# Kernel optimization log

Measured on AMD Instinct MI355X. Metric: run time of the kernel, lower is better.

The kernel has to match this reference:

```python
import jax, jax.numpy as jnp
import numpy as np

N = 8192
TEMP = 0.5
EPS = 1e-12


def _normalize(z):
    # F.normalize(z, p=2, dim=1): x / max(||x||, eps)
    n = jnp.sqrt(jnp.sum(z * z, axis=1, keepdims=True))
    return z / jnp.maximum(n, EPS)


def _gcn(edge_index, edge_weight, x, w, b):
    # torch.sparse.mm(adj, x @ w): out[row] += adj[row, col] * support[col]
    support = x @ w
    msg = support[edge_index[1]] * edge_weight[:, None]
    return jax.ops.segment_sum(msg, edge_index[0], num_segments=N) + b


def _encoder(edge_index, edge_weight, feat, w_l1a, b_l1a, w_l1b, b_l1b, w_g1, b_g1, w_g2, b_g2):
    x = jax.nn.relu(feat @ w_l1a + b_l1a) @ w_l1b + b_l1b  # [N, 32]
    h = jax.nn.relu(_gcn(edge_index, edge_weight, x, w_g1, b_g1))  # [N, hid]
    return _gcn(edge_index, edge_weight, h, w_g2, b_g2)  # [N, act_fn]


def _proj(h, w_fc1, b_fc1, w_fc2, b_fc2):
    return jax.nn.elu(h @ w_fc1 + b_fc1) @ w_fc2 + b_fc2


def _loss(z1, z2):
    z1n = _normalize(z1)
    z2n = _normalize(z2)
    refl = jnp.exp((z1n @ z1n.T) / TEMP)      # [N, N]
    between = jnp.exp((z1n @ z2n.T) / TEMP)   # [N, N]
    denom = refl.sum(1) + between.sum(1) - jnp.diagonal(refl)
    return -jnp.log(jnp.diagonal(between) / denom)


def setup_inputs() -> dict:
    key = jax.random.key(0)
    ks = jax.random.split(key, 20)
    E = 262144
    in_dim, hid_dim, act_fn, out_dim = 512, 256, 128, 64

    def kaiming(k, shape):
        fan_in = shape[0]
        bound = np.sqrt(6.0 / fan_in)
        return jax.random.uniform(k, shape, jnp.float32, -bound, bound)

    return {
        "feat1": jax.random.normal(ks[0], (N, in_dim), jnp.float32),
        "feat2": jax.random.normal(ks[1], (N, in_dim), jnp.float32),
        "edge_index1": jax.random.randint(ks[2], (2, E), 0, N, jnp.int32),
        "edge_weight1": jax.random.uniform(ks[3], (E,), jnp.float32),
        "edge_index2": jax.random.randint(ks[4], (2, E), 0, N, jnp.int32),
        "edge_weight2": jax.random.uniform(ks[5], (E,), jnp.float32),
        "w_l1a": kaiming(ks[6], (in_dim, 64)),
        "b_l1a": jnp.zeros((64,), jnp.float32),
        "w_l1b": kaiming(ks[7], (64, 32)),
        "b_l1b": jnp.zeros((32,), jnp.float32),
        "w_g1": kaiming(ks[8], (32, hid_dim)),
        "b_g1": jnp.zeros((hid_dim,), jnp.float32),
        "w_g2": kaiming(ks[9], (hid_dim, act_fn)),
        "b_g2": jnp.zeros((act_fn,), jnp.float32),
        "w_fc1": kaiming(ks[10], (act_fn, out_dim)),
        "b_fc1": jnp.zeros((out_dim,), jnp.float32),
        "w_fc2": kaiming(ks[11], (out_dim, act_fn)),
        "b_fc2": jnp.zeros((act_fn,), jnp.float32),
    }


def reference(feat1, feat2, edge_index1, edge_weight1, edge_index2, edge_weight2,
              w_l1a, b_l1a, w_l1b, b_l1b, w_g1, b_g1, w_g2, b_g2,
              w_fc1, b_fc1, w_fc2, b_fc2):
    h1 = _encoder(edge_index1, edge_weight1, feat1, w_l1a, b_l1a, w_l1b, b_l1b, w_g1, b_g1, w_g2, b_g2)
    h2 = _encoder(edge_index2, edge_weight2, feat2, w_l1a, b_l1a, w_l1b, b_l1b, w_g1, b_g1, w_g2, b_g2)
    z1 = _proj(h1, w_fc1, b_fc1, w_fc2, b_fc2)
    z2 = _proj(h2, w_fc1, b_fc1, w_fc2, b_fc2)
    l1 = _loss(z1, z2)
    l2 = _loss(z2, z1)
    return ((l1 + l2) * 0.5).mean()
```

## Files before the change

### kernel.cpp

```cpp
#include <hip/hip_runtime.h>
#include <hip/hip_bf16.h>
#include <math.h>


#define NROWS 8192
#define MROWS 16384
#define NEDGE 262144

typedef __attribute__((ext_vector_type(8))) short bf16x8;
typedef __attribute__((ext_vector_type(4))) float f32x4;
typedef __attribute__((ext_vector_type(2))) float f32x2;
typedef long long i64;

__device__ __forceinline__ short f2bf(float f){
  union { float f; unsigned u; } cv; cv.f = f;
  unsigned u = cv.u;
  unsigned r = (u + 0x7fffu + ((u >> 16) & 1u)) >> 16;
  return (short)r;
}
__device__ __forceinline__ f32x4 mfma16(bf16x8 a, bf16x8 b, f32x4 c){
  return __builtin_amdgcn_mfma_f32_16x16x32_bf16(a, b, c, 0, 0, 0);
}
__device__ __forceinline__ float fexp2(float x){
#if __has_builtin(__builtin_amdgcn_exp2f)
  return __builtin_amdgcn_exp2f(x);
#else
  return exp2f(x);
#endif
}

__device__ unsigned char f2e4m3_sw(float f){
  float a = fabsf(f);
  unsigned s = (__float_as_uint(f)>>24)&0x80u;
  if (!(a>0.f)) return (unsigned char)s;
  if (a>448.f) a=448.f;
  int e; frexpf(a,&e);
  int eff=e-1;
  unsigned code;
  if (eff<-6){
    float q=rintf(a*512.f);
    code=(unsigned)q; if(code>7)code=7;
  } else {
    float q=rintf(a*exp2f((float)(3-eff)));
    unsigned mant=(unsigned)q;
    if(mant>=16){mant=8;eff++;}
    if(eff>8) return (unsigned char)(s|0x7e);
    code=((unsigned)(eff+7)<<3)|(mant-8);
  }
  return (unsigned char)(s|code);
}
__device__ __forceinline__ unsigned short pack2fp8(float a, float b){
#if __has_builtin(__builtin_amdgcn_cvt_pk_fp8_f32)
  int v = __builtin_amdgcn_cvt_pk_fp8_f32(a, b, 0, false);
  return (unsigned short)(v & 0xffff);
#else
  return (unsigned short)((unsigned)f2e4m3_sw(a) | ((unsigned)f2e4m3_sw(b)<<8));
#endif
}

struct WtArgs {
  const float* src[6];
  short* dst[6];
  int K[6], N[6];
  int off[7];
  int nwt;
};
__global__ void setup_k(WtArgs a, const int* __restrict__ ei1, const int* __restrict__ ei2,
                        int* __restrict__ deg1, int* __restrict__ deg2){
  int b = blockIdx.x;
  if (b < a.nwt){
    int i = b*256 + threadIdx.x;
    if (i >= a.off[6]) return;
    int s = 0;
    #pragma unroll
    for (int j=1;j<6;j++) if (i >= a.off[j]) s=j;
    int l = i - a.off[s];
    int K=a.K[s], N=a.N[s];
    int k=l/N, n=l-k*N;
    a.dst[s][(long)n*K+k] = f2bf(a.src[s][l]);
  } else {
    int hb = b - a.nwt;
    const int* ei = (hb < NEDGE/256) ? ei1 : ei2;
    int* deg = (hb < NEDGE/256) ? deg1 : deg2;
    int e = (hb % (NEDGE/256))*256 + threadIdx.x;
    atomicAdd(&deg[ei[e]], 1);
  }
}

__global__ __launch_bounds__(256) void mlp12_k(const float* __restrict__ F0, const float* __restrict__ F1,
                                               const short* __restrict__ Wa, const float* __restrict__ ba,
                                               const short* __restrict__ Wb, const float* __restrict__ bb,
                                               short* __restrict__ xb){
  __shared__ short As[32*520];
  __shared__ short a1s[32*72];
  const int tid = threadIdx.x;
  const int m0 = blockIdx.x*32;
  const float* F = (m0 < NROWS) ? (F0 + (long)m0*512) : (F1 + (long)(m0-NROWS)*512);
  {
    float4 st[16];
    #pragma unroll
    for (int i=0;i<16;i++) st[i] = *(const float4*)(F + (long)(i*256+tid)*4);
    #pragma unroll
    for (int i=0;i<16;i++){
      int idx = i*256+tid, row = idx>>7, c4 = idx&127;
      unsigned lo = (unsigned)(unsigned short)f2bf(st[i].x) | ((unsigned)(unsigned short)f2bf(st[i].y)<<16);
      unsigned hi = (unsigned)(unsigned short)f2bf(st[i].z) | ((unsigned)(unsigned short)f2bf(st[i].w)<<16);
      uint2 o = {lo, hi};
      *(uint2*)&As[row*520 + c4*4] = o;
    }
  }
  __syncthreads();
  const int wave = tid>>6, lane = tid&63, quad = lane>>4, cl = lane&15;
  f32x4 zero = {0.f,0.f,0.f,0.f};
  {
    const int wno = wave*16;
    f32x4 acc[2] = {zero, zero};
    #pragma unroll
    for (int kc=0;kc<16;kc++){
      const int ko = kc*32 + quad*8;
      bf16x8 a0 = *(const bf16x8*)&As[(cl)*520 + ko];
      bf16x8 a1 = *(const bf16x8*)&As[(16+cl)*520 + ko];
      bf16x8 b = *(const bf16x8*)(Wa + (long)(wno + cl)*512 + ko);
      acc[0] = mfma16(a0, b, acc[0]);
      acc[1] = mfma16(a1, b, acc[1]);
    }
    int col = wno + cl;
    float bv = ba[col];
    #pragma unroll
    for (int mt=0;mt<2;mt++)
      #pragma unroll
      for (int r=0;r<4;r++)
        a1s[(mt*16 + quad*4 + r)*72 + col] = f2bf(fmaxf(acc[mt][r] + bv, 0.f));
  }
  __syncthreads();
  if (wave < 2){
    f32x4 acc2[2] = {zero, zero};
    #pragma unroll
    for (int kc=0;kc<2;kc++){
      const int ko = kc*32 + quad*8;
      bf16x8 a = *(const bf16x8*)&a1s[(wave*16+cl)*72 + ko];
      #pragma unroll
      for (int nt=0;nt<2;nt++){
        bf16x8 b = *(const bf16x8*)(Wb + (long)(nt*16 + cl)*64 + ko);
        acc2[nt] = mfma16(a, b, acc2[nt]);
      }
    }
    #pragma unroll
    for (int nt=0;nt<2;nt++){
      int col = nt*16 + cl;
      float bv = bb[col];
      #pragma unroll
      for (int r=0;r<4;r++)
        xb[(long)(m0 + wave*16 + quad*4 + r)*32 + col] = f2bf(acc2[nt][r] + bv);
    }
  }
}

__global__ void scan2_k(const int* __restrict__ deg1, int* __restrict__ rs1, int* __restrict__ cur1,
                        const int* __restrict__ deg2, int* __restrict__ rs2, int* __restrict__ cur2){
  const int* deg = blockIdx.x ? deg2 : deg1;
  int* rowstart = blockIdx.x ? rs2 : rs1;
  int* cursor = blockIdx.x ? cur2 : cur1;
  __shared__ int wsum[4];
  int t = threadIdx.x;
  int lane = t & 63, wv = t >> 6;
  int loc[32];
  int s = 0;
  for (int j=0;j<32;j++){ int d = deg[t*32+j]; loc[j] = s; s += d; }
  int v = s;
  #pragma unroll
  for (int m=1;m<64;m<<=1){
    int o = __shfl_up(v, m);
    if (lane >= m) v += o;
  }
  if (lane==63) wsum[wv] = v;
  __syncthreads();
  int woff = 0;
  for (int w=0; w<wv; w++) woff += wsum[w];
  int excl = v + woff - s;
  for (int j=0;j<32;j++){ int x = excl + loc[j]; rowstart[t*32+j]=x; cursor[t*32+j]=x; }
  if (t==255) rowstart[NROWS] = excl + s;
}
__global__ void fill2_k(const int* __restrict__ ei1, const float* __restrict__ w1, int* __restrict__ cur1,
                        int* __restrict__ ecol1, float* __restrict__ ew1,
                        const int* __restrict__ ei2, const float* __restrict__ w2, int* __restrict__ cur2,
                        int* __restrict__ ecol2, float* __restrict__ ew2){
  int b = blockIdx.x;
  bool g2 = (b >= NEDGE/256);
  const int* ei = g2 ? ei2 : ei1;
  const float* w = g2 ? w2 : w1;
  int* cursor = g2 ? cur2 : cur1;
  int* ecol = g2 ? ecol2 : ecol1;
  float* ew = g2 ? ew2 : ew1;
  int e = (b % (NEDGE/256))*256 + threadIdx.x;
  int r = ei[e];
  int p = atomicAdd(&cursor[r], 1);
  ecol[p] = ei[NEDGE + e];
  ew[p] = w[e];
}

__device__ __forceinline__ void acc8(float* acc, int4 v, float f){
  const unsigned* u = (const unsigned*)&v;
  #pragma unroll
  for (int i=0;i<4;i++){
    union{unsigned x; float y;} lo, hi;
    lo.x = u[i] << 16;
    hi.x = u[i] & 0xffff0000u;
    acc[2*i]   = fmaf(f, lo.y, acc[2*i]);
    acc[2*i+1] = fmaf(f, hi.y, acc[2*i+1]);
  }
}
template<int C>
__device__ __forceinline__ void gather_row(float* acc, const short* sb,
                                           const int* ec, const float* w, int s, int e){
  int k = s;
  for (; k+16 <= e; k+=16){
    int c[16]; float f[16]; int4 v[16];
    #pragma unroll
    for (int u=0;u<16;u++){ c[u]=ec[k+u]; f[u]=w[k+u]; }
    #pragma unroll
    for (int u=0;u<16;u++) v[u] = *(const int4*)(sb + (long)c[u]*C);
    #pragma unroll
    for (int u=0;u<16;u++) acc8(acc, v[u], f[u]);
  }
  for (; k+4 <= e; k+=4){
    int c0=ec[k],c1=ec[k+1],c2=ec[k+2],c3=ec[k+3];
    float f0=w[k],f1=w[k+1],f2=w[k+2],f3=w[k+3];
    int4 v0 = *(const int4*)(sb + (long)c0*C);
    int4 v1 = *(const int4*)(sb + (long)c1*C);
    int4 v2 = *(const int4*)(sb + (long)c2*C);
    int4 v3 = *(const int4*)(sb + (long)c3*C);
    acc8(acc,v0,f0); acc8(acc,v1,f1); acc8(acc,v2,f2); acc8(acc,v3,f3);
  }
  for (; k < e; k++){
    int4 v0 = *(const int4*)(sb + (long)ec[k]*C);
    acc8(acc,v0,w[k]);
  }
}

template<int C, bool RELU, bool HASB>
__global__ __launch_bounds__(256) void gather_k(const short* __restrict__ sup,
    const int* __restrict__ rs1, const int* __restrict__ ec1, const float* __restrict__ w1,
    const int* __restrict__ rs2, const int* __restrict__ ec2, const float* __restrict__ w2,
    const float* __restrict__ bias, short* __restrict__ out){
  constexpr int G = C/8;
  const int g = threadIdx.x % G;
  const int sub = threadIdx.x / G;
  const int row = blockIdx.x*(256/G) + sub;
  const int* rs; const int* ec; const float* w; int soff, lr;
  if (row < NROWS){ rs=rs1; ec=ec1; w=w1; soff=0; lr=row; }
  else            { rs=rs2; ec=ec2; w=w2; soff=NROWS; lr=row-NROWS; }
  const short* sb = sup + (long)soff*C + g*8;
  float acc[8];
  #pragma unroll
  for (int j=0;j<8;j++) acc[j] = HASB ? bias[g*8+j] : 0.f;
  gather_row<C>(acc, sb, ec, w, rs[lr], rs[lr+1]);
  int4 ov;
  unsigned* ou = (unsigned*)&ov;
  #pragma unroll
  for (int i=0;i<4;i++){
    float a0 = acc[2*i], a1 = acc[2*i+1];
    if (RELU){ a0 = fmaxf(a0,0.f); a1 = fmaxf(a1,0.f); }
    ou[i] = (unsigned)(unsigned short)f2bf(a0) | ((unsigned)(unsigned short)f2bf(a1)<<16);
  }
  *(int4*)(out + (long)row*C + g*8) = ov;
}

__global__ __launch_bounds__(256) void gg_k(const short* __restrict__ xb,
    const int* __restrict__ rs1, const int* __restrict__ ec1, const float* __restrict__ w1,
    const int* __restrict__ rs2, const int* __restrict__ ec2, const float* __restrict__ w2,
    const short* __restrict__ Wg1, const float* __restrict__ bg1,
    const short* __restrict__ Wg2, short* __restrict__ s2){
  __shared__ short axs[64*40];
  __shared__ short hbs[64*264];
  const int tid = threadIdx.x;
  const int m0 = blockIdx.x*64;
  {
    const int g = tid & 3, sub = tid >> 2;
    const int row = m0 + sub;
    const int* rs; const int* ec; const float* w; int soff, lr;
    if (row < NROWS){ rs=rs1; ec=ec1; w=w1; soff=0; lr=row; }
    else            { rs=rs2; ec=ec2; w=w2; soff=NROWS; lr=row-NROWS; }
    const short* sb = xb + (long)soff*32 + g*8;
    float acc[8];
    #pragma unroll
    for (int j=0;j<8;j++) acc[j] = 0.f;
    gather_row<32>(acc, sb, ec, w, rs[lr], rs[lr+1]);
    int4 ov;
    unsigned* ou = (unsigned*)&ov;
    #pragma unroll
    for (int i=0;i<4;i++)
      ou[i] = (unsigned)(unsigned short)f2bf(acc[2*i]) | ((unsigned)(unsigned short)f2bf(acc[2*i+1])<<16);
    *(int4*)&axs[sub*40 + g*8] = ov;
  }
  __syncthreads();
  const int wave = tid>>6, lane = tid&63, quad = lane>>4, cl = lane&15;
  f32x4 zero = {0.f,0.f,0.f,0.f};
  {
    const int wno = wave*64;
    f32x4 acc[4][4];
    #pragma unroll
    for (int i=0;i<4;i++)
      #pragma unroll
      for (int j=0;j<4;j++) acc[i][j]=zero;
    const int ko = quad*8;
    bf16x8 a[4], b[4];
    #pragma unroll
    for (int mt=0;mt<4;mt++)
      a[mt] = *(const bf16x8*)&axs[(mt*16+cl)*40 + ko];
    #pragma unroll
    for (int nt=0;nt<4;nt++)
      b[nt] = *(const bf16x8*)(Wg1 + (long)(wno + nt*16 + cl)*32 + ko);
    #pragma unroll
    for (int mt=0;mt<4;mt++)
      #pragma unroll
      for (int nt=0;nt<4;nt++)
        acc[mt][nt] = mfma16(a[mt], b[nt], acc[mt][nt]);
    #pragma unroll
    for (int nt=0;nt<4;nt++){
      int col = wno + nt*16 + cl;
      float bv = bg1[col];
      #pragma unroll
      for (int mt=0;mt<4;mt++)
        #pragma unroll
        for (int r=0;r<4;r++)
          hbs[(mt*16 + quad*4 + r)*264 + col] = f2bf(fmaxf(acc[mt][nt][r] + bv, 0.f));
    }
  }
  __syncthreads();
  {
    const int wno = wave*32;
    f32x4 acc[4][2];
    #pragma unroll
    for (int i=0;i<4;i++){ acc[i][0]=zero; acc[i][1]=zero; }
    #pragma unroll
    for (int kc=0;kc<8;kc++){
      const int ko = kc*32 + quad*8;
      bf16x8 a[4], b[2];
      #pragma unroll
      for (int mt=0;mt<4;mt++)
        a[mt] = *(const bf16x8*)&hbs[(mt*16+cl)*264 + ko];
      #pragma unroll
      for (int nt=0;nt<2;nt++)
        b[nt] = *(const bf16x8*)(Wg2 + (long)(wno + nt*16 + cl)*256 + ko);
      #pragma unroll
      for (int mt=0;mt<4;mt++)
        #pragma unroll
        for (int nt=0;nt<2;nt++)
          acc[mt][nt] = mfma16(a[mt], b[nt], acc[mt][nt]);
    }
    #pragma unroll
    for (int mt=0;mt<4;mt++)
      #pragma unroll
      for (int nt=0;nt<2;nt++){
        int col = wno + nt*16 + cl;
        #pragma unroll
        for (int r=0;r<4;r++)
          s2[(long)(m0 + mt*16 + quad*4 + r)*128 + col] = f2bf(acc[mt][nt][r]);
      }
  }
}

__global__ __launch_bounds__(256) void pn_k(const short* __restrict__ hh,
    const short* __restrict__ Wf1, const float* __restrict__ bf1,
    const short* __restrict__ Wf2, const float* __restrict__ bf2,
    unsigned short* __restrict__ Zf, float* __restrict__ bdot){
  __shared__ short hs[64*136];
  __shared__ short t2s[64*72];
  __shared__ float zs[64*132];
  __shared__ float sp[4][64];
  __shared__ float dp[4][32];
  __shared__ float rnS[64];
  const float SQKE = 1.6986436f;
  const int tid = threadIdx.x;
  const int wave = tid>>6, lane = tid&63, quad = lane>>4, cl = lane&15;
  const int m0h = blockIdx.x*32;
  {
    const short* r1 = hh + (long)m0h*128;
    const short* r2 = hh + (long)(NROWS + m0h)*128;
    #pragma unroll
    for (int i=0;i<2;i++){
      int idx = i*256 + tid;
      int row = idx >> 4, c16 = idx & 15;
      *(int4*)&hs[row*136 + c16*8] = *(const int4*)(r1 + row*128 + c16*8);
      *(int4*)&hs[(32+row)*136 + c16*8] = *(const int4*)(r2 + row*128 + c16*8);
    }
  }
  __syncthreads();
  f32x4 zero = {0.f,0.f,0.f,0.f};
  {
    const int wno = wave*16;
    f32x4 acc[4];
    #pragma unroll
    for (int i=0;i<4;i++) acc[i]=zero;
    #pragma unroll
    for (int kc=0;kc<4;kc++){
      const int ko = kc*32 + quad*8;
      bf16x8 a[4], b;
      #pragma unroll
      for (int mt=0;mt<4;mt++)
        a[mt] = *(const bf16x8*)&hs[(mt*16+cl)*136 + ko];
      b = *(const bf16x8*)(Wf1 + (long)(wno + cl)*128 + ko);
      #pragma unroll
      for (int mt=0;mt<4;mt++) acc[mt] = mfma16(a[mt], b, acc[mt]);
    }
    int col = wno + cl;
    float bv = bf1[col];
    #pragma unroll
    for (int mt=0;mt<4;mt++)
      #pragma unroll
      for (int r=0;r<4;r++){
        float v = acc[mt][r] + bv;
        v = (v > 0.f) ? v : expm1f(v);
        t2s[(mt*16 + quad*4 + r)*72 + col] = f2bf(v);
      }
  }
  __syncthreads();
  {
    const int wno = wave*32;
    f32x4 acc[4][2];
    #pragma unroll
    for (int i=0;i<4;i++){ acc[i][0]=zero; acc[i][1]=zero; }
    #pragma unroll
    for (int kc=0;kc<2;kc++){
      const int ko = kc*32 + quad*8;
      bf16x8 a[4], b[2];
      #pragma unroll
      for (int mt=0;mt<4;mt++)
        a[mt] = *(const bf16x8*)&t2s[(mt*16+cl)*72 + ko];
      #pragma unroll
      for (int nt=0;nt<2;nt++)
        b[nt] = *(const bf16x8*)(Wf2 + (long)(wno + nt*16 + cl)*64 + ko);
      #pragma unroll
      for (int mt=0;mt<4;mt++)
        #pragma unroll
        for (int nt=0;nt<2;nt++)
          acc[mt][nt] = mfma16(a[mt], b[nt], acc[mt][nt]);
    }
    #pragma unroll
    for (int mt=0;mt<4;mt++)
      #pragma unroll
      for (int nt=0;nt<2;nt++){
        int col = wno + nt*16 + cl;
        float bv = bf2[col];
        #pragma unroll
        for (int r=0;r<4;r++)
          zs[(mt*16 + quad*4 + r)*132 + col] = acc[mt][nt][r] + bv;
      }
  }
  __syncthreads();
  {
    int row = tid & 63, qtr = tid >> 6;
    const float* zr = &zs[row*132 + qtr*32];
    float s = 0.f;
    #pragma unroll 8
    for (int c=0;c<32;c++) s += zr[c]*zr[c];
    sp[qtr][row] = s;
    if (row < 32){
      const float* zb_ = &zs[(row+32)*132 + qtr*32];
      float d = 0.f;
      #pragma unroll 8
      for (int c=0;c<32;c++) d += zr[c]*zb_[c];
      dp[qtr][row] = d;
    }
  }
  __syncthreads();
  if (tid < 64){
    float ssq = sp[0][tid]+sp[1][tid]+sp[2][tid]+sp[3][tid];
    rnS[tid] = 1.f / fmaxf(sqrtf(ssq), 1e-12f);
  }
  __syncthreads();
  if (tid < 32){
    float dot = dp[0][tid]+dp[1][tid]+dp[2][tid]+dp[3][tid];
    bdot[m0h + tid] = dot * rnS[tid] * rnS[tid+32];
  }
  {
    int lr = tid >> 2;
    int grow = (lr < 32) ? (m0h + lr) : (NROWS + m0h + lr - 32);
    float s = rnS[lr] * SQKE;
    int p0 = (tid & 3)*16;
    #pragma unroll
    for (int pp=0;pp<16;pp++){
      int p = p0 + pp;
      int d = p>>1, h = p&1, kc = d>>3, q = (d>>1)&3, j4 = d&1;
      long o = ((long)(grow>>4)*512 + kc*128 + j4 + ((grow&15)+16*q)*2)*2 + h;
      Zf[o] = pack2fp8(zs[lr*132 + 2*p]*s, zs[lr*132 + 2*p + 1]*s);
    }
  }
}

__global__ __launch_bounds__(256,4) void gram3_k(const unsigned char* __restrict__ Zf,
                                                 float* __restrict__ P){
  __shared__ float srow[4][64];
  __shared__ float scol[4][64];
  const int wave = threadIdx.x>>6, lane = threadIdx.x&63;
  const int t = blockIdx.x*4 + wave;
  int ti = (int)((513.0f - sqrtf(513.0f*513.0f - 8.0f*(float)t))*0.5f);
  while ((ti+1)*256 - ((ti+1)*ti)/2 <= t) ti++;
  while (ti*256 - (ti*(ti-1))/2 > t) ti--;
  const int tj = ti + (t - (ti*256 - (ti*(ti-1))/2));
  const unsigned char* za = Zf + (long)ti*16*512 + lane*8;
  const unsigned char* zb = Zf + (long)tj*16*512 + lane*8;

  f32x4 zero = {0.f,0.f,0.f,0.f};
  f32x4 acc[4][4];
  #pragma unroll
  for (int i=0;i<4;i++)
    #pragma unroll
    for (int j=0;j<4;j++) acc[i][j]=zero;

  i64 aA[4], bA[4], aB[4], bB[4];
  #pragma unroll
  for (int x=0;x<4;x++){
    aA[x] = *(const i64*)(za + (x*4+0)*512);
    bA[x] = *(const i64*)(zb + (x*4+0)*512);
  }
  #pragma unroll
  for (int kc=0;kc<4;kc++){
    i64* ac = (kc&1) ? aB : aA;
    i64* bc = (kc&1) ? bB : bA;
    i64* an = (kc&1) ? aA : aB;
    i64* bn = (kc&1) ? bA : bB;
    if (kc<3){
      #pragma unroll
      for (int x=0;x<4;x++){
        an[x] = *(const i64*)(za + (x*4+kc+1)*512);
        bn[x] = *(const i64*)(zb + (x*4+kc+1)*512);
      }
    }
    #pragma unroll
    for (int mt=0;mt<4;mt++)
      #pragma unroll
      for (int nt=0;nt<4;nt++)
        acc[mt][nt] = __builtin_amdgcn_mfma_f32_16x16x32_fp8_fp8(ac[mt], bc[nt], acc[mt][nt], 0, 0, 0);
  }

  const int quad = lane>>4, cl = lane&15;
  f32x2 z2 = {0.f,0.f};
  f32x2 rs01[4] = {z2,z2,z2,z2}, rs23[4] = {z2,z2,z2,z2};
  f32x2 cs[4] = {z2,z2,z2,z2};
  #pragma unroll
  for (int mt=0;mt<4;mt++){
    #pragma unroll
    for (int nt=0;nt<4;nt++){
      f32x4 v = acc[mt][nt];
      float e0 = fexp2(v[0]), e1 = fexp2(v[1]);
      float e2 = fexp2(v[2]), e3 = fexp2(v[3]);
      f32x2 p01 = {e0,e1}, p23 = {e2,e3};
      rs01[mt] += p01; rs23[mt] += p23;
      cs[nt] += p01; cs[nt] += p23;
    }
  }
  #pragma unroll
  for (int mt=0;mt<4;mt++){
    union{f32x2 v; double d;} u0, u1;
    u0.v = rs01[mt]; u1.v = rs23[mt];
    #pragma unroll
    for (int m=1;m<16;m<<=1){
      union{double d; f32x2 v;} o0, o1;
      o0.d = __shfl_xor(u0.d, m); o1.d = __shfl_xor(u1.d, m);
      u0.v += o0.v; u1.v += o1.v;
    }
    if (cl==0){
      f32x4 rv = {u0.v.x, u0.v.y, u1.v.x, u1.v.y};
      *(f32x4*)&srow[wave][mt*16 + quad*4] = rv;
    }
  }
  __threadfence_block();
  P[((long)ti*256 + tj)*64 + lane] = srow[wave][lane];
  if (ti != tj){
    #pragma unroll
    for (int nt=0;nt<4;nt++){
      float s = cs[nt].x + cs[nt].y;
      s += __shfl_xor(s,16); s += __shfl_xor(s,32);
      if (quad==0) scol[wave][nt*16 + cl] = s;
    }
    __threadfence_block();
    P[((long)tj*256 + ti)*64 + lane] = scol[wave][lane];
  }
}

__global__ __launch_bounds__(256) void rloss_k(const float* __restrict__ P,
                                               const float* __restrict__ bdot,
                                               float* __restrict__ out){
  __shared__ float s1p[4][64];
  __shared__ float s2p[4][64];
  __shared__ float red[64];
  const float E2 = 7.3890560989306495f;
  const int a = blockIdx.x;
  const int t = threadIdx.x;
  const int r = t & 63, bq = t >> 6;
  const float* P1 = P + (long)a*16384;
  const float* P2 = P + (long)(a+128)*16384;
  float s1 = 0.f, s2 = 0.f;
  for (int b = bq; b < 256; b += 4){
    s1 += P1[b*64 + r];
    s2 += P2[b*64 + r];
  }
  s1p[bq][r] = s1; s2p[bq][r] = s2;
  __syncthreads();
  if (t < 64){
    float S1 = s1p[0][t]+s1p[1][t]+s1p[2][t]+s1p[3][t];
    float S2 = s2p[0][t]+s2p[1][t]+s2p[2][t]+s2p[3][t];
    int i = a*64 + t;
    float lb = 2.f * bdot[i];
    float v = 0.5f * ((logf(S1 - E2) - lb) + (logf(S2 - E2) - lb));
    #pragma unroll
    for (int m=1;m<64;m<<=1) v += __shfl_xor(v, m);
    if (t==0) atomicAdd(out, v / (float)NROWS);
  }
}

extern "C" void kernel_launch(void* const* d_in, const int* in_sizes, int n_in,
                              void* d_out, int out_size, void* d_ws, size_t ws_size,
                              hipStream_t stream){
  const float* feat1 = (const float*)d_in[0];
  const float* feat2 = (const float*)d_in[1];
  const int*   ei1   = (const int*)d_in[2];
  const float* w1    = (const float*)d_in[3];
  const int*   ei2   = (const int*)d_in[4];
  const float* w2    = (const float*)d_in[5];
  const float* w_l1a = (const float*)d_in[6];
  const float* b_l1a = (const float*)d_in[7];
  const float* w_l1b = (const float*)d_in[8];
  const float* b_l1b = (const float*)d_in[9];
  const float* w_g1  = (const float*)d_in[10];
  const float* b_g1  = (const float*)d_in[11];
  const float* w_g2  = (const float*)d_in[12];
  const float* b_g2  = (const float*)d_in[13];
  const float* w_fc1 = (const float*)d_in[14];
  const float* b_fc1 = (const float*)d_in[15];
  const float* w_fc2 = (const float*)d_in[16];
  const float* b_fc2 = (const float*)d_in[17];

  float* P = (float*)d_ws;
  char* base = (char*)d_ws;
  size_t off = (size_t)17<<20;
  auto alloc = [&](size_t bytes)->void*{
    void* r = base + off;
    off = (off + bytes + 255) & ~(size_t)255;
    return r;
  };
  short* xb   = (short*)alloc((size_t)MROWS*32*2);
  short* s2   = (short*)alloc((size_t)MROWS*128*2);
  short* hh   = (short*)alloc((size_t)MROWS*128*2);
  short* wl1a_t = (short*)alloc(512*64*2);
  short* wl1b_t = (short*)alloc(64*32*2);
  short* wg1_t  = (short*)alloc(32*256*2);
  short* wg2_t  = (short*)alloc(256*128*2);
  short* wfc1_t = (short*)alloc(128*64*2);
  short* wfc2_t = (short*)alloc(64*128*2);
  unsigned short* Zf = (unsigned short*)alloc((size_t)MROWS*128);
  int*   deg1 = (int*)alloc(NROWS*4);
  int*   deg2 = (int*)alloc(NROWS*4);
  int* rs1  = (int*)alloc((NROWS+1)*4);
  int* cur1 = (int*)alloc(NROWS*4);
  int* rs2  = (int*)alloc((NROWS+1)*4);
  int* cur2 = (int*)alloc(NROWS*4);
  int*   ecol1 = (int*)alloc((size_t)NEDGE*4);
  float* ewt1  = (float*)alloc((size_t)NEDGE*4);
  int*   ecol2 = (int*)alloc((size_t)NEDGE*4);
  float* ewt2  = (float*)alloc((size_t)NEDGE*4);
  float* bdot  = (float*)alloc(NROWS*4);

  hipMemsetAsync(deg1, 0, (size_t)2*NROWS*4, stream);
  hipMemsetAsync(d_out, 0, sizeof(float), stream);

  WtArgs wa;
  wa.src[0]=w_l1a; wa.dst[0]=wl1a_t; wa.K[0]=512; wa.N[0]=64;
  wa.src[1]=w_l1b; wa.dst[1]=wl1b_t; wa.K[1]=64;  wa.N[1]=32;
  wa.src[2]=w_g1;  wa.dst[2]=wg1_t;  wa.K[2]=32;  wa.N[2]=256;
  wa.src[3]=w_g2;  wa.dst[3]=wg2_t;  wa.K[3]=256; wa.N[3]=128;
  wa.src[4]=w_fc1; wa.dst[4]=wfc1_t; wa.K[4]=128; wa.N[4]=64;
  wa.src[5]=w_fc2; wa.dst[5]=wfc2_t; wa.K[5]=64;  wa.N[5]=128;
  wa.off[0]=0;
  for (int i=0;i<6;i++) wa.off[i+1] = wa.off[i] + wa.K[i]*wa.N[i];
  wa.nwt = (wa.off[6]+255)/256;

  setup_k<<<wa.nwt + 2*(NEDGE/256),256,0,stream>>>(wa, ei1, ei2, deg1, deg2);
  scan2_k<<<2,256,0,stream>>>(deg1, rs1, cur1, deg2, rs2, cur2);
  fill2_k<<<2*(NEDGE/256),256,0,stream>>>(ei1, w1, cur1, ecol1, ewt1,
                                          ei2, w2, cur2, ecol2, ewt2);

  mlp12_k<<<MROWS/32,256,0,stream>>>(feat1, feat2, wl1a_t, b_l1a, wl1b_t, b_l1b, xb);
  gg_k<<<MROWS/64,256,0,stream>>>(xb, rs1,ecol1,ewt1, rs2,ecol2,ewt2,
                                  wg1_t, b_g1, wg2_t, s2);
  gather_k<128,false,true><<<MROWS/16,256,0,stream>>>(s2, rs1,ecol1,ewt1,
                                                      rs2,ecol2,ewt2, b_g2, hh);
  pn_k<<<NROWS/32,256,0,stream>>>(hh, wfc1_t, b_fc1, wfc2_t, b_fc2, Zf, bdot);

  gram3_k<<<8224,256,0,stream>>>((const unsigned char*)Zf, P);
  rloss_k<<<128,256,0,stream>>>(P, bdot, (float*)d_out);
}
```

Baseline: 273.1 us.

## Fold fc1 weight into second GCN layer to gather 64-wide instead of 128

Uses associativity: (A·(h·Wg2)+bg2)·Wfc1 = A·(h·(Wg2·Wfc1)) + (bg2·Wfc1+bf1). The combined weight and bias are precomputed in the scan kernel, so the second sparse gather moves 64-wide rows instead of 128-wide, and the fc1 matmul in the projection kernel is replaced by a bias add plus ELU. This halves gather traffic and removes one GEMM stage. In exchange the combined weight is rounded to bf16, which changes numerics slightly.

```diff
diff --git a/kernel.cpp b/kernel.cpp
--- a/kernel.cpp
+++ b/kernel.cpp
@@ -12,6 +12,9 @@
 typedef __attribute__((ext_vector_type(2))) float f32x2;
 typedef long long i64;
 
+__device__ __forceinline__ float bf2f(short s){
+  union { unsigned u; float f; } cv; cv.u = ((unsigned)(unsigned short)s) << 16; return cv.f;
+}
 __device__ __forceinline__ short f2bf(float f){
   union { float f; unsigned u; } cv; cv.f = f;
   unsigned u = cv.u;
@@ -157,29 +160,53 @@
 }
 
 __global__ void scan2_k(const int* __restrict__ deg1, int* __restrict__ rs1, int* __restrict__ cur1,
-                        const int* __restrict__ deg2, int* __restrict__ rs2, int* __restrict__ cur2){
-  const int* deg = blockIdx.x ? deg2 : deg1;
-  int* rowstart = blockIdx.x ? rs2 : rs1;
-  int* cursor = blockIdx.x ? cur2 : cur1;
-  __shared__ int wsum[4];
+                        const int* __restrict__ deg2, int* __restrict__ rs2, int* __restrict__ cur2,
+                        const short* __restrict__ wg2_t, const short* __restrict__ wfc1_t,
+                        short* __restrict__ Wc_t,
+                        const float* __restrict__ bg2, const float* __restrict__ bf1,
+                        float* __restrict__ bc){
+  int b = blockIdx.x;
   int t = threadIdx.x;
-  int lane = t & 63, wv = t >> 6;
-  int loc[32];
-  int s = 0;
-  for (int j=0;j<32;j++){ int d = deg[t*32+j]; loc[j] = s; s += d; }
-  int v = s;
-  #pragma unroll
-  for (int m=1;m<64;m<<=1){
-    int o = __shfl_up(v, m);
-    if (lane >= m) v += o;
-  }
-  if (lane==63) wsum[wv] = v;
-  __syncthreads();
-  int woff = 0;
-  for (int w=0; w<wv; w++) woff += wsum[w];
-  int excl = v + woff - s;
-  for (int j=0;j<32;j++){ int x = excl + loc[j]; rowstart[t*32+j]=x; cursor[t*32+j]=x; }
-  if (t==255) rowstart[NROWS] = excl + s;
+  if (b < 2){
+    const int* deg = b ? deg2 : deg1;
+    int* rowstart = b ? rs2 : rs1;
+    int* cursor = b ? cur2 : cur1;
+    __shared__ int wsum[4];
+    int lane = t & 63, wv = t >> 6;
+    int loc[32];
+    int s = 0;
+    for (int j=0;j<32;j++){ int d = deg[t*32+j]; loc[j] = s; s += d; }
+    int v = s;
+    #pragma unroll
+    for (int m=1;m<64;m<<=1){
+      int o = __shfl_up(v, m);
+      if (lane >= m) v += o;
+    }
+    if (lane==63) wsum[wv] = v;
+    __syncthreads();
+    int woff = 0;
+    for (int w=0; w<wv; w++) woff += wsum[w];
+    int excl = v + woff - s;
+    for (int j=0;j<32;j++){ int x = excl + loc[j]; rowstart[t*32+j]=x; cursor[t*32+j]=x; }
+    if (t==255) rowstart[NROWS] = excl + s;
+  } else if (b < 18){
+    int e0 = (b-2)*1024 + t*4;
+    #pragma unroll
+    for (int u=0;u<4;u++){
+      int e = e0 + u;
+      int n = e >> 8, k = e & 255;
+      float s = 0.f;
+      for (int j=0;j<128;j++)
+        s += bf2f(wfc1_t[n*128+j]) * bf2f(wg2_t[j*256+k]);
+      Wc_t[n*256+k] = f2bf(s);
+    }
+  } else {
+    if (t < 64){
+      float s = bf1[t];
+      for (int j=0;j<128;j++) s += bg2[j]*bf2f(wfc1_t[t*128+j]);
+      bc[t] = s;
+    }
+  }
 }
 __global__ void fill2_k(const int* __restrict__ ei1, const float* __restrict__ w1, int* __restrict__ cur1,
                         int* __restrict__ ecol1, float* __restrict__ ew1,
@@ -270,7 +297,7 @@
     const int* __restrict__ rs1, const int* __restrict__ ec1, const float* __restrict__ w1,
     const int* __restrict__ rs2, const int* __restrict__ ec2, const float* __restrict__ w2,
     const short* __restrict__ Wg1, const float* __restrict__ bg1,
-    const short* __restrict__ Wg2, short* __restrict__ s2){
+    const short* __restrict__ Wc, short* __restrict__ s2){
   __shared__ short axs[64*40];
   __shared__ short hbs[64*264];
   const int tid = threadIdx.x;
@@ -329,44 +356,34 @@
   }
   __syncthreads();
   {
-    const int wno = wave*32;
-    f32x4 acc[4][2];
-    #pragma unroll
-    for (int i=0;i<4;i++){ acc[i][0]=zero; acc[i][1]=zero; }
+    const int wno = wave*16;
+    f32x4 acc[4];
+    #pragma unroll
+    for (int i=0;i<4;i++) acc[i]=zero;
     #pragma unroll
     for (int kc=0;kc<8;kc++){
       const int ko = kc*32 + quad*8;
-      bf16x8 a[4], b[2];
-      #pragma unroll
-      for (int mt=0;mt<4;mt++)
-        a[mt] = *(const bf16x8*)&hbs[(mt*16+cl)*264 + ko];
-      #pragma unroll
-      for (int nt=0;nt<2;nt++)
-        b[nt] = *(const bf16x8*)(Wg2 + (long)(wno + nt*16 + cl)*256 + ko);
-      #pragma unroll
-      for (int mt=0;mt<4;mt++)
-        #pragma unroll
-        for (int nt=0;nt<2;nt++)
-          acc[mt][nt] = mfma16(a[mt], b[nt], acc[mt][nt]);
-    }
+      bf16x8 b = *(const bf16x8*)(Wc + (long)(wno + cl)*256 + ko);
+      #pragma unroll
+      for (int mt=0;mt<4;mt++){
+        bf16x8 a = *(const bf16x8*)&hbs[(mt*16+cl)*264 + ko];
+        acc[mt] = mfma16(a, b, acc[mt]);
+      }
+    }
+    int col = wno + cl;
     #pragma unroll
     for (int mt=0;mt<4;mt++)
       #pragma unroll
-      for (int nt=0;nt<2;nt++){
-        int col = wno + nt*16 + cl;
-        #pragma unroll
-        for (int r=0;r<4;r++)
-          s2[(long)(m0 + mt*16 + quad*4 + r)*128 + col] = f2bf(acc[mt][nt][r]);
-      }
-  }
-}
-
-__global__ __launch_bounds__(256) void pn_k(const short* __restrict__ hh,
-    const short* __restrict__ Wf1, const float* __restrict__ bf1,
+      for (int r=0;r<4;r++)
+        s2[(long)(m0 + mt*16 + quad*4 + r)*64 + col] = f2bf(acc[mt][r]);
+  }
+}
+
+__global__ __launch_bounds__(256) void pn_k(const short* __restrict__ ax2,
+    const float* __restrict__ bc,
     const short* __restrict__ Wf2, const float* __restrict__ bf2,
     unsigned short* __restrict__ Zf, float* __restrict__ bdot){
-  __shared__ short hs[64*136];
-  __shared__ short t2s[64*72];
+  __shared__ short hs[64*72];
   __shared__ float zs[64*132];
   __shared__ float sp[4][64];
   __shared__ float dp[4][32];
@@ -376,46 +393,28 @@
   const int wave = tid>>6, lane = tid&63, quad = lane>>4, cl = lane&15;
   const int m0h = blockIdx.x*32;
   {
-    const short* r1 = hh + (long)m0h*128;
-    const short* r2 = hh + (long)(NROWS + m0h)*128;
     #pragma unroll
     for (int i=0;i<2;i++){
       int idx = i*256 + tid;
-      int row = idx >> 4, c16 = idx & 15;
-      *(int4*)&hs[row*136 + c16*8] = *(const int4*)(r1 + row*128 + c16*8);
-      *(int4*)&hs[(32+row)*136 + c16*8] = *(const int4*)(r2 + row*128 + c16*8);
+      int row = idx >> 3, c8 = idx & 7;
+      int grow = (row < 32) ? (m0h + row) : (NROWS + m0h + row - 32);
+      int4 v = *(const int4*)(ax2 + (long)grow*64 + c8*8);
+      const short* sv = (const short*)&v;
+      int4 ov;
+      unsigned* ou = (unsigned*)&ov;
+      #pragma unroll
+      for (int p=0;p<4;p++){
+        float x0 = bf2f(sv[2*p])   + bc[c8*8 + 2*p];
+        float x1 = bf2f(sv[2*p+1]) + bc[c8*8 + 2*p + 1];
+        x0 = (x0 > 0.f) ? x0 : expm1f(x0);
+        x1 = (x1 > 0.f) ? x1 : expm1f(x1);
+        ou[p] = (unsigned)(unsigned short)f2bf(x0) | ((unsigned)(unsigned short)f2bf(x1)<<16);
+      }
+      *(int4*)&hs[row*72 + c8*8] = ov;
     }
   }
   __syncthreads();
   f32x4 zero = {0.f,0.f,0.f,0.f};
-  {
-    const int wno = wave*16;
-    f32x4 acc[4];
-    #pragma unroll
-    for (int i=0;i<4;i++) acc[i]=zero;
-    #pragma unroll
-    for (int kc=0;kc<4;kc++){
-      const int ko = kc*32 + quad*8;
-      bf16x8 a[4], b;
-      #pragma unroll
-      for (int mt=0;mt<4;mt++)
-        a[mt] = *(const bf16x8*)&hs[(mt*16+cl)*136 + ko];
-      b = *(const bf16x8*)(Wf1 + (long)(wno + cl)*128 + ko);
-      #pragma unroll
-      for (int mt=0;mt<4;mt++) acc[mt] = mfma16(a[mt], b, acc[mt]);
-    }
-    int col = wno + cl;
-    float bv = bf1[col];
-    #pragma unroll
-    for (int mt=0;mt<4;mt++)
-      #pragma unroll
-      for (int r=0;r<4;r++){
-        float v = acc[mt][r] + bv;
-        v = (v > 0.f) ? v : expm1f(v);
-        t2s[(mt*16 + quad*4 + r)*72 + col] = f2bf(v);
-      }
-  }
-  __syncthreads();
   {
     const int wno = wave*32;
     f32x4 acc[4][2];
@@ -427,7 +426,7 @@
       bf16x8 a[4], b[2];
       #pragma unroll
       for (int mt=0;mt<4;mt++)
-        a[mt] = *(const bf16x8*)&t2s[(mt*16+cl)*72 + ko];
+        a[mt] = *(const bf16x8*)&hs[(mt*16+cl)*72 + ko];
       #pragma unroll
       for (int nt=0;nt<2;nt++)
         b[nt] = *(const bf16x8*)(Wf2 + (long)(wno + nt*16 + cl)*64 + ko);
@@ -518,7 +517,7 @@
   #pragma unroll
   for (int kc=0;kc<4;kc++){
     i64* ac = (kc&1) ? aB : aA;
-    i64* bc = (kc&1) ? bB : bA;
+    i64* bc_ = (kc&1) ? bB : bA;
     i64* an = (kc&1) ? aA : aB;
     i64* bn = (kc&1) ? bA : bB;
     if (kc<3){
@@ -532,7 +531,7 @@
     for (int mt=0;mt<4;mt++)
       #pragma unroll
       for (int nt=0;nt<4;nt++)
-        acc[mt][nt] = __builtin_amdgcn_mfma_f32_16x16x32_fp8_fp8(ac[mt], bc[nt], acc[mt][nt], 0, 0, 0);
+        acc[mt][nt] = __builtin_amdgcn_mfma_f32_16x16x32_fp8_fp8(ac[mt], bc_[nt], acc[mt][nt], 0, 0, 0);
   }
 
   const int quad = lane>>4, cl = lane&15;
@@ -585,7 +584,6 @@
                                                float* __restrict__ out){
   __shared__ float s1p[4][64];
   __shared__ float s2p[4][64];
-  __shared__ float red[64];
   const float E2 = 7.3890560989306495f;
   const int a = blockIdx.x;
   const int t = threadIdx.x;
@@ -642,14 +640,16 @@
     return r;
   };
   short* xb   = (short*)alloc((size_t)MROWS*32*2);
-  short* s2   = (short*)alloc((size_t)MROWS*128*2);
-  short* hh   = (short*)alloc((size_t)MROWS*128*2);
+  short* s2   = (short*)alloc((size_t)MROWS*64*2);
+  short* ax2  = (short*)alloc((size_t)MROWS*64*2);
   short* wl1a_t = (short*)alloc(512*64*2);
   short* wl1b_t = (short*)alloc(64*32*2);
   short* wg1_t  = (short*)alloc(32*256*2);
   short* wg2_t  = (short*)alloc(256*128*2);
   short* wfc1_t = (short*)alloc(128*64*2);
   short* wfc2_t = (short*)alloc(64*128*2);
+  short* Wc_t   = (short*)alloc(64*256*2);
+  float* bc     = (float*)alloc(64*4);
   unsigned short* Zf = (unsigned short*)alloc((size_t)MROWS*128);
   int*   deg1 = (int*)alloc(NROWS*4);
   int*   deg2 = (int*)alloc(NROWS*4);
@@ -678,16 +678,17 @@
   wa.nwt = (wa.off[6]+255)/256;
 
   setup_k<<<wa.nwt + 2*(NEDGE/256),256,0,stream>>>(wa, ei1, ei2, deg1, deg2);
-  scan2_k<<<2,256,0,stream>>>(deg1, rs1, cur1, deg2, rs2, cur2);
+  scan2_k<<<19,256,0,stream>>>(deg1, rs1, cur1, deg2, rs2, cur2,
+                               wg2_t, wfc1_t, Wc_t, b_g2, b_fc1, bc);
   fill2_k<<<2*(NEDGE/256),256,0,stream>>>(ei1, w1, cur1, ecol1, ewt1,
                                           ei2, w2, cur2, ecol2, ewt2);
 
   mlp12_k<<<MROWS/32,256,0,stream>>>(feat1, feat2, wl1a_t, b_l1a, wl1b_t, b_l1b, xb);
   gg_k<<<MROWS/64,256,0,stream>>>(xb, rs1,ecol1,ewt1, rs2,ecol2,ewt2,
-                                  wg1_t, b_g1, wg2_t, s2);
-  gather_k<128,false,true><<<MROWS/16,256,0,stream>>>(s2, rs1,ecol1,ewt1,
-                                                      rs2,ecol2,ewt2, b_g2, hh);
-  pn_k<<<NROWS/32,256,0,stream>>>(hh, wfc1_t, b_fc1, wfc2_t, b_fc2, Zf, bdot);
+                                  wg1_t, b_g1, Wc_t, s2);
+  gather_k<64,false,false><<<MROWS/32,256,0,stream>>>(s2, rs1,ecol1,ewt1,
+                                                      rs2,ecol2,ewt2, nullptr, ax2);
+  pn_k<<<NROWS/32,256,0,stream>>>(ax2, bc, wfc2_t, b_fc2, Zf, bdot);
 
   gram3_k<<<8224,256,0,stream>>>((const unsigned char*)Zf, P);
   rloss_k<<<128,256,0,stream>>>(P, bdot, (float*)d_out);
```

After: 298.1 us. +9.1%, slower.
